# Optimization experiments

Hardware: AMD Instinct MI355X
Metric: run time of the kernel (lower is better)

## Reference

```python
import jax, jax.numpy as jnp
import numpy as np

NUM_HEADS = 4
HEAD_DIM = 32  # out_dim 128 / 4 heads


def setup_inputs() -> dict:
    key = jax.random.key(0)
    ks = jax.random.split(key, 8)
    N, E, R, D = 40000, 640000, 64, 128
    return {
        "entity_emb": jax.random.normal(ks[0], (N, D), jnp.float32),
        "relation_emb": jax.random.normal(ks[1], (R, D), jnp.float32),
        "edge_index": jax.random.randint(ks[2], (2, E), 0, N, jnp.int64),
        "edge_type": jax.random.randint(ks[3], (E,), 0, R, jnp.int64),
        "W": jax.random.normal(ks[4], (D, D), jnp.float32) / np.sqrt(D),
        "W_r": jax.random.normal(ks[5], (D, D), jnp.float32) / np.sqrt(D),
        "attn_w": jax.random.normal(ks[6], (3 * HEAD_DIM, 1), jnp.float32) / np.sqrt(3 * HEAD_DIM),
        "attn_b": jnp.zeros((1,), jnp.float32),
    }


def reference(entity_emb, relation_emb, edge_index, edge_type, W, W_r, attn_w, attn_b):
    N = entity_emb.shape[0]
    H, HD = NUM_HEADS, HEAD_DIM
    # projections (PyTorch Linear: x @ W.T)
    h = (entity_emb @ W.T).reshape(N, H, HD)
    r = relation_emb @ W_r.T
    src, dst = edge_index[0], edge_index[1]
    h_src = h[src]                                    # [E, H, HD]
    h_dst = h[dst]
    r_edge = r[edge_type].reshape(-1, H, HD)
    attn_in = jnp.concatenate([h_src, r_edge, h_dst], axis=-1)  # [E, H, 3*HD]
    scores = jax.nn.leaky_relu(attn_in @ attn_w[:, 0] + attn_b[0], negative_slope=0.2)  # [E, H]
    scores = jnp.exp(scores - jnp.max(scores))
    attn_sum = jax.ops.segment_sum(scores, dst, num_segments=N)  # [N, H]
    attn_weights = scores / (attn_sum[dst] + 1e-8)               # dropout is identity in eval
    msg = attn_weights[..., None] * h_src                        # [E, H, HD]
    out = jax.ops.segment_sum(msg, dst, num_segments=N)          # [N, H, HD]
    return out.reshape(N, H * HD)
```

## Files before the change

kernel.cpp:

```cpp
#include <hip/hip_runtime.h>
#include <math.h>

#define HEADS 4
#define DIM 128
#define CAP 128

typedef __bf16 bf16x8 __attribute__((ext_vector_type(8)));
typedef float f32x4 __attribute__((ext_vector_type(4)));

__device__ __forceinline__ unsigned short f2bf(float x) {
    unsigned u = __float_as_uint(x);
    unsigned r = (u + 0x7FFFu + ((u >> 16) & 1u)) >> 16;
    return (unsigned short)r;
}
__device__ __forceinline__ float bf2f(unsigned short v) {
    return __uint_as_float(((unsigned)v) << 16);
}

__global__ __launch_bounds__(256) void k_cvtW(const float* __restrict__ W,
                                              unsigned short* __restrict__ W16) {
    int j = blockIdx.x * 256 + threadIdx.x;
    float4 v = ((const float4*)W)[j];
    ushort4 us;
    us.x = f2bf(v.x); us.y = f2bf(v.y); us.z = f2bf(v.z); us.w = f2bf(v.w);
    ((ushort4*)W16)[j] = us;
}

__global__ __launch_bounds__(256) void k_proj(const float* __restrict__ ent,
                                              const unsigned short* __restrict__ W16,
                                              const float* __restrict__ aw,
                                              const int* __restrict__ ei,
                                              const int* __restrict__ et,
                                              unsigned short* __restrict__ h16,
                                              float4* __restrict__ s1,
                                              float4* __restrict__ s3,
                                              int* __restrict__ cnt,
                                              int* __restrict__ packed,
                                              int N, int E, int NBR) {
    int t = threadIdx.x;
    int bid = blockIdx.x;
    if (bid >= NBR) {
        int EB = gridDim.x - NBR;
        int eb = bid - NBR;
        int per = (E + EB - 1) / EB;
        int e0 = eb * per;
        int e1 = e0 + per;
        if (e1 > E) e1 = E;
        for (int e = e0 + t; e < e1; e += 256) {
            int dn = ei[E + e];
            int pos = atomicAdd(&cnt[dn], 1);
            if (pos >= CAP) pos = CAP - 1;
            packed[(size_t)dn * CAP + pos] = (ei[e] << 6) | et[e];
        }
        return;
    }
    int wv = t >> 6, lane = t & 63, ln = lane & 15, quad = lane >> 4;
    int er = bid * 64 + wv * 16 + ln;
    int erc = er < N ? er : N - 1;
    const float4* ent4 = (const float4*)ent;
    bf16x8 bfr[4];
#pragma unroll
    for (int ks = 0; ks < 4; ++ks) {
        float4 a0 = ent4[(size_t)erc * 32 + ks * 8 + quad * 2];
        float4 a1 = ent4[(size_t)erc * 32 + ks * 8 + quad * 2 + 1];
        bf16x8 f;
        f[0] = (__bf16)a0.x; f[1] = (__bf16)a0.y; f[2] = (__bf16)a0.z; f[3] = (__bf16)a0.w;
        f[4] = (__bf16)a1.x; f[5] = (__bf16)a1.y; f[6] = (__bf16)a1.z; f[7] = (__bf16)a1.w;
        bfr[ks] = f;
    }
    f32x4 acc[8];
#pragma unroll
    for (int mt = 0; mt < 8; ++mt) acc[mt] = (f32x4){0.f, 0.f, 0.f, 0.f};
#pragma unroll
    for (int ks = 0; ks < 4; ++ks) {
#pragma unroll
        for (int mt = 0; mt < 8; ++mt) {
            bf16x8 afr = *(const bf16x8*)&W16[(mt * 16 + ln) * DIM + ks * 32 + quad * 8];
            acc[mt] = __builtin_amdgcn_mfma_f32_16x16x32_bf16(afr, bfr[ks], acc[mt], 0, 0, 0);
        }
    }
    const float4* awv = (const float4*)aw;
    float s1h[4] = {0.f, 0.f, 0.f, 0.f}, s3h[4] = {0.f, 0.f, 0.f, 0.f};
#pragma unroll
    for (int mt = 0; mt < 8; ++mt) {
        int d0 = mt * 16 + quad * 4;
        if (er < N) {
            ushort4 us;
            us.x = f2bf(acc[mt][0]); us.y = f2bf(acc[mt][1]);
            us.z = f2bf(acc[mt][2]); us.w = f2bf(acc[mt][3]);
            *(ushort4*)&h16[(size_t)er * DIM + d0] = us;
        }
        int wi = (mt & 1) * 4 + quad;
        float4 w1 = awv[wi], w3 = awv[16 + wi];
        int hh = mt >> 1;
        s1h[hh] += acc[mt][0] * w1.x + acc[mt][1] * w1.y + acc[mt][2] * w1.z + acc[mt][3] * w1.w;
        s3h[hh] += acc[mt][0] * w3.x + acc[mt][1] * w3.y + acc[mt][2] * w3.z + acc[mt][3] * w3.w;
    }
#pragma unroll
    for (int hh = 0; hh < HEADS; ++hh) {
        s1h[hh] += __shfl_xor(s1h[hh], 16);
        s1h[hh] += __shfl_xor(s1h[hh], 32);
        s3h[hh] += __shfl_xor(s3h[hh], 16);
        s3h[hh] += __shfl_xor(s3h[hh], 32);
    }
    if (quad == 0 && er < N) {
        s1[er] = make_float4(s1h[0], s1h[1], s1h[2], s1h[3]);
        s3[er] = make_float4(s3h[0], s3h[1], s3h[2], s3h[3]);
    }
}

__global__ __launch_bounds__(256) void k_s2(const float* __restrict__ rel,
                                            const float* __restrict__ Wr,
                                            const float* __restrict__ aw,
                                            float* __restrict__ s2, int RH) {
    __shared__ float v[DIM * HEADS];
    int t = threadIdx.x;
    for (int i = t; i < DIM * HEADS; i += 256) {
        int k = i >> 2, hh = i & 3;
        float a = 0.f;
        for (int j = 0; j < 32; ++j) a += Wr[(hh * 32 + j) * DIM + k] * aw[32 + j];
        v[i] = a;
    }
    __syncthreads();
    int o = blockIdx.x * 4 + (t >> 6);
    if (o >= RH) return;
    int r = o >> 2, hh = o & 3;
    int l = t & 63;
    float p = rel[r * DIM + l] * v[l * 4 + hh] + rel[r * DIM + 64 + l] * v[(64 + l) * 4 + hh];
#pragma unroll
    for (int off = 32; off > 0; off >>= 1) p += __shfl_down(p, off);
    if (l == 0) s2[o] = p;
}

__global__ __launch_bounds__(64) void k_out(const int* __restrict__ packed,
                                            const int* __restrict__ cnt,
                                            const float4* __restrict__ s1,
                                            const float4* __restrict__ s2,
                                            const float4* __restrict__ s3,
                                            const float* __restrict__ ab,
                                            const unsigned short* __restrict__ h16,
                                            float* __restrict__ out, int N) {
    __shared__ int src_l[64];
    __shared__ float es_l[64 * 4];
    int n = blockIdx.x;
    int t = threadIdx.x;
    int hh = t >> 4;
    float b = ab[0];
    float4 s3n = s3[n];
    int beg = n * CAP;
    int c = cnt[n];
    if (c > CAP) c = CAP;
    float a0 = 0.f, a1 = 0.f, sum = 0.f;
    for (int base = 0; base < c; base += 64) {
        int m = c - base;
        if (m > 64) m = 64;
        __syncthreads();
        if (t < m) {
            int p = packed[beg + base + t];
            int s = p >> 6, ty = p & 63;
            float4 a = s1[s], cc = s2[ty];
            float4 sc;
            sc.x = a.x + cc.x + s3n.x + b;
            sc.y = a.y + cc.y + s3n.y + b;
            sc.z = a.z + cc.z + s3n.z + b;
            sc.w = a.w + cc.w + s3n.w + b;
            sc.x = sc.x > 0.f ? sc.x : 0.2f * sc.x;
            sc.y = sc.y > 0.f ? sc.y : 0.2f * sc.y;
            sc.z = sc.z > 0.f ? sc.z : 0.2f * sc.z;
            sc.w = sc.w > 0.f ? sc.w : 0.2f * sc.w;
            src_l[t] = s;
            es_l[t * 4 + 0] = __expf(sc.x);
            es_l[t * 4 + 1] = __expf(sc.y);
            es_l[t * 4 + 2] = __expf(sc.z);
            es_l[t * 4 + 3] = __expf(sc.w);
        }
        __syncthreads();
        int i = 0;
        for (; i + 4 <= m; i += 4) {
            int q0 = src_l[i], q1 = src_l[i + 1], q2 = src_l[i + 2], q3 = src_l[i + 3];
            float e0 = es_l[i * 4 + hh], e1 = es_l[(i + 1) * 4 + hh];
            float e2 = es_l[(i + 2) * 4 + hh], e3 = es_l[(i + 3) * 4 + hh];
            unsigned v0 = *(const unsigned*)&h16[(size_t)q0 * DIM + 2 * t];
            unsigned v1 = *(const unsigned*)&h16[(size_t)q1 * DIM + 2 * t];
            unsigned v2 = *(const unsigned*)&h16[(size_t)q2 * DIM + 2 * t];
            unsigned v3 = *(const unsigned*)&h16[(size_t)q3 * DIM + 2 * t];
            sum += (e0 + e1) + (e2 + e3);
            a0 += e0 * bf2f((unsigned short)v0);
            a1 += e0 * bf2f((unsigned short)(v0 >> 16));
            a0 += e1 * bf2f((unsigned short)v1);
            a1 += e1 * bf2f((unsigned short)(v1 >> 16));
            a0 += e2 * bf2f((unsigned short)v2);
            a1 += e2 * bf2f((unsigned short)(v2 >> 16));
            a0 += e3 * bf2f((unsigned short)v3);
            a1 += e3 * bf2f((unsigned short)(v3 >> 16));
        }
        for (; i < m; ++i) {
            int s = src_l[i];
            float e = es_l[i * 4 + hh];
            unsigned v = *(const unsigned*)&h16[(size_t)s * DIM + 2 * t];
            sum += e;
            a0 += e * bf2f((unsigned short)v);
            a1 += e * bf2f((unsigned short)(v >> 16));
        }
    }
    float inv = 1.f / (sum + 1e-8f);
    *(float2*)&out[(size_t)n * DIM + 2 * t] = make_float2(a0 * inv, a1 * inv);
}

extern "C" void kernel_launch(void* const* d_in, const int* in_sizes, int n_in,
                              void* d_out, int out_size, void* d_ws, size_t ws_size,
                              hipStream_t stream) {
    const float* ent = (const float*)d_in[0];
    const float* rel = (const float*)d_in[1];
    const int* ei = (const int*)d_in[2];
    const int* et = (const int*)d_in[3];
    const float* W = (const float*)d_in[4];
    const float* Wr = (const float*)d_in[5];
    const float* aw = (const float*)d_in[6];
    const float* ab = (const float*)d_in[7];

    int N = in_sizes[0] / DIM;
    int R = in_sizes[1] / DIM;
    int E = in_sizes[3];
    int NBR = (N + 63) / 64;
    int EB = 1875;

    char* w = (char*)d_ws;
    unsigned short* W16 = (unsigned short*)w;   w += (size_t)DIM * DIM * 2;
    unsigned short* h16 = (unsigned short*)w;   w += ((size_t)N * DIM * 2 + 15) / 16 * 16;
    float* s1 = (float*)w;     w += (size_t)N * HEADS * 4;
    float* s3 = (float*)w;     w += (size_t)N * HEADS * 4;
    float* s2 = (float*)w;     w += ((size_t)R * HEADS * 4 + 15) / 16 * 16;
    int* cnt = (int*)w;        w += (size_t)N * 4;
    int* packed = (int*)w;     w += (size_t)N * CAP * 4;

    float* out = (float*)d_out;

    (void)hipMemsetAsync(cnt, 0, (size_t)N * 4, stream);

    k_cvtW<<<16, 256, 0, stream>>>(W, W16);
    k_proj<<<NBR + EB, 256, 0, stream>>>(ent, W16, aw, ei, et, h16, (float4*)s1,
                                         (float4*)s3, cnt, packed, N, E, NBR);
    k_s2<<<(R * HEADS + 3) / 4, 256, 0, stream>>>(rel, Wr, aw, s2, R * HEADS);
    k_out<<<N, 64, 0, stream>>>(packed, cnt, (const float4*)s1, (const float4*)s2,
                                (const float4*)s3, ab, h16, out, N);
}
```

Measured before the change: 162.6 us.

## Split per-destination edge buckets into eight sub-buckets to cut atomic contention

Edge bucketing now spreads each destination's edges over 8 sub-buckets chosen by block index, each with its own counter and a capacity of 32. Each bucketing block handles a fixed 1024 edges, issuing four loads per thread before its atomics. The output kernel gathers the sub-buckets through a prefix over their counts into shared memory and does one pass with a single barrier. This aims to reduce same-address atomic contention and raise memory-level parallelism, at the cost of 8x larger counter and bucket buffers (more memset and scattered reads) and truncation if one sub-bucket receives more than 32 edges.

```diff
diff --git a/kernel.cpp b/kernel.cpp
--- a/kernel.cpp
+++ b/kernel.cpp
@@ -3,7 +3,8 @@
 
 #define HEADS 4
 #define DIM 128
-#define CAP 128
+#define NG 8
+#define CAPG 32
 
 typedef __bf16 bf16x8 __attribute__((ext_vector_type(8)));
 typedef float f32x4 __attribute__((ext_vector_type(4)));
@@ -40,18 +41,29 @@
     int t = threadIdx.x;
     int bid = blockIdx.x;
     if (bid >= NBR) {
-        int EB = gridDim.x - NBR;
+        int g = bid & (NG - 1);
         int eb = bid - NBR;
-        int per = (E + EB - 1) / EB;
-        int e0 = eb * per;
-        int e1 = e0 + per;
-        if (e1 > E) e1 = E;
-        for (int e = e0 + t; e < e1; e += 256) {
-            int dn = ei[E + e];
-            int pos = atomicAdd(&cnt[dn], 1);
-            if (pos >= CAP) pos = CAP - 1;
-            packed[(size_t)dn * CAP + pos] = (ei[e] << 6) | et[e];
+        int e0 = eb * 1024;
+        int dn[4], pk[4];
+        bool vl[4];
+#pragma unroll
+        for (int j = 0; j < 4; ++j) {
+            int e = e0 + j * 256 + t;
+            vl[j] = e < E;
+            int ec = vl[j] ? e : 0;
+            dn[j] = ei[E + ec];
+            pk[j] = (ei[ec] << 6) | et[ec];
         }
+        int pos[4];
+#pragma unroll
+        for (int j = 0; j < 4; ++j)
+            if (vl[j]) pos[j] = atomicAdd(&cnt[(size_t)g * N + dn[j]], 1);
+#pragma unroll
+        for (int j = 0; j < 4; ++j)
+            if (vl[j]) {
+                int p = pos[j] < CAPG ? pos[j] : CAPG - 1;
+                packed[((size_t)g * N + dn[j]) * CAPG + p] = pk[j];
+            }
         return;
     }
     int wv = t >> 6, lane = t & 63, ln = lane & 15, quad = lane >> 4;
@@ -140,68 +152,74 @@
                                             const float* __restrict__ ab,
                                             const unsigned short* __restrict__ h16,
                                             float* __restrict__ out, int N) {
-    __shared__ int src_l[64];
-    __shared__ float es_l[64 * 4];
+    __shared__ int src_l[NG * CAPG];
+    __shared__ float es_l[NG * CAPG * 4];
     int n = blockIdx.x;
     int t = threadIdx.x;
     int hh = t >> 4;
     float b = ab[0];
     float4 s3n = s3[n];
-    int beg = n * CAP;
-    int c = cnt[n];
-    if (c > CAP) c = CAP;
+    int cg[NG], pf[NG];
+    int tot = 0;
+#pragma unroll
+    for (int g = 0; g < NG; ++g) {
+        int c = cnt[(size_t)g * N + n];
+        if (c > CAPG) c = CAPG;
+        cg[g] = c;
+        pf[g] = tot;
+        tot += c;
+    }
+    for (int p = t; p < tot; p += 64) {
+        int g = 0;
+#pragma unroll
+        for (int gg = 1; gg < NG; ++gg)
+            if (p >= pf[gg]) g = gg;
+        int pk = packed[((size_t)g * N + n) * CAPG + (p - pf[g])];
+        int s = pk >> 6, ty = pk & 63;
+        float4 a = s1[s], cc = s2[ty];
+        float4 sc;
+        sc.x = a.x + cc.x + s3n.x + b;
+        sc.y = a.y + cc.y + s3n.y + b;
+        sc.z = a.z + cc.z + s3n.z + b;
+        sc.w = a.w + cc.w + s3n.w + b;
+        sc.x = sc.x > 0.f ? sc.x : 0.2f * sc.x;
+        sc.y = sc.y > 0.f ? sc.y : 0.2f * sc.y;
+        sc.z = sc.z > 0.f ? sc.z : 0.2f * sc.z;
+        sc.w = sc.w > 0.f ? sc.w : 0.2f * sc.w;
+        src_l[p] = s;
+        es_l[p * 4 + 0] = __expf(sc.x);
+        es_l[p * 4 + 1] = __expf(sc.y);
+        es_l[p * 4 + 2] = __expf(sc.z);
+        es_l[p * 4 + 3] = __expf(sc.w);
+    }
+    __syncthreads();
     float a0 = 0.f, a1 = 0.f, sum = 0.f;
-    for (int base = 0; base < c; base += 64) {
-        int m = c - base;
-        if (m > 64) m = 64;
-        __syncthreads();
-        if (t < m) {
-            int p = packed[beg + base + t];
-            int s = p >> 6, ty = p & 63;
-            float4 a = s1[s], cc = s2[ty];
-            float4 sc;
-            sc.x = a.x + cc.x + s3n.x + b;
-            sc.y = a.y + cc.y + s3n.y + b;
-            sc.z = a.z + cc.z + s3n.z + b;
-            sc.w = a.w + cc.w + s3n.w + b;
-            sc.x = sc.x > 0.f ? sc.x : 0.2f * sc.x;
-            sc.y = sc.y > 0.f ? sc.y : 0.2f * sc.y;
-            sc.z = sc.z > 0.f ? sc.z : 0.2f * sc.z;
-            sc.w = sc.w > 0.f ? sc.w : 0.2f * sc.w;
-            src_l[t] = s;
-            es_l[t * 4 + 0] = __expf(sc.x);
-            es_l[t * 4 + 1] = __expf(sc.y);
-            es_l[t * 4 + 2] = __expf(sc.z);
-            es_l[t * 4 + 3] = __expf(sc.w);
-        }
-        __syncthreads();
-        int i = 0;
-        for (; i + 4 <= m; i += 4) {
-            int q0 = src_l[i], q1 = src_l[i + 1], q2 = src_l[i + 2], q3 = src_l[i + 3];
-            float e0 = es_l[i * 4 + hh], e1 = es_l[(i + 1) * 4 + hh];
-            float e2 = es_l[(i + 2) * 4 + hh], e3 = es_l[(i + 3) * 4 + hh];
-            unsigned v0 = *(const unsigned*)&h16[(size_t)q0 * DIM + 2 * t];
-            unsigned v1 = *(const unsigned*)&h16[(size_t)q1 * DIM + 2 * t];
-            unsigned v2 = *(const unsigned*)&h16[(size_t)q2 * DIM + 2 * t];
-            unsigned v3 = *(const unsigned*)&h16[(size_t)q3 * DIM + 2 * t];
-            sum += (e0 + e1) + (e2 + e3);
-            a0 += e0 * bf2f((unsigned short)v0);
-            a1 += e0 * bf2f((unsigned short)(v0 >> 16));
-            a0 += e1 * bf2f((unsigned short)v1);
-            a1 += e1 * bf2f((unsigned short)(v1 >> 16));
-            a0 += e2 * bf2f((unsigned short)v2);
-            a1 += e2 * bf2f((unsigned short)(v2 >> 16));
-            a0 += e3 * bf2f((unsigned short)v3);
-            a1 += e3 * bf2f((unsigned short)(v3 >> 16));
-        }
-        for (; i < m; ++i) {
-            int s = src_l[i];
-            float e = es_l[i * 4 + hh];
-            unsigned v = *(const unsigned*)&h16[(size_t)s * DIM + 2 * t];
-            sum += e;
-            a0 += e * bf2f((unsigned short)v);
-            a1 += e * bf2f((unsigned short)(v >> 16));
-        }
+    int i = 0;
+    for (; i + 4 <= tot; i += 4) {
+        int q0 = src_l[i], q1 = src_l[i + 1], q2 = src_l[i + 2], q3 = src_l[i + 3];
+        float e0 = es_l[i * 4 + hh], e1 = es_l[(i + 1) * 4 + hh];
+        float e2 = es_l[(i + 2) * 4 + hh], e3 = es_l[(i + 3) * 4 + hh];
+        unsigned v0 = *(const unsigned*)&h16[(size_t)q0 * DIM + 2 * t];
+        unsigned v1 = *(const unsigned*)&h16[(size_t)q1 * DIM + 2 * t];
+        unsigned v2 = *(const unsigned*)&h16[(size_t)q2 * DIM + 2 * t];
+        unsigned v3 = *(const unsigned*)&h16[(size_t)q3 * DIM + 2 * t];
+        sum += (e0 + e1) + (e2 + e3);
+        a0 += e0 * bf2f((unsigned short)v0);
+        a1 += e0 * bf2f((unsigned short)(v0 >> 16));
+        a0 += e1 * bf2f((unsigned short)v1);
+        a1 += e1 * bf2f((unsigned short)(v1 >> 16));
+        a0 += e2 * bf2f((unsigned short)v2);
+        a1 += e2 * bf2f((unsigned short)(v2 >> 16));
+        a0 += e3 * bf2f((unsigned short)v3);
+        a1 += e3 * bf2f((unsigned short)(v3 >> 16));
+    }
+    for (; i < tot; ++i) {
+        int s = src_l[i];
+        float e = es_l[i * 4 + hh];
+        unsigned v = *(const unsigned*)&h16[(size_t)s * DIM + 2 * t];
+        sum += e;
+        a0 += e * bf2f((unsigned short)v);
+        a1 += e * bf2f((unsigned short)(v >> 16));
     }
     float inv = 1.f / (sum + 1e-8f);
     *(float2*)&out[(size_t)n * DIM + 2 * t] = make_float2(a0 * inv, a1 * inv);
@@ -223,7 +241,7 @@
     int R = in_sizes[1] / DIM;
     int E = in_sizes[3];
     int NBR = (N + 63) / 64;
-    int EB = 1875;
+    int EB = (E + 1023) / 1024;
 
     char* w = (char*)d_ws;
     unsigned short* W16 = (unsigned short*)w;   w += (size_t)DIM * DIM * 2;
@@ -231,12 +249,12 @@
     float* s1 = (float*)w;     w += (size_t)N * HEADS * 4;
     float* s3 = (float*)w;     w += (size_t)N * HEADS * 4;
     float* s2 = (float*)w;     w += ((size_t)R * HEADS * 4 + 15) / 16 * 16;
-    int* cnt = (int*)w;        w += (size_t)N * 4;
-    int* packed = (int*)w;     w += (size_t)N * CAP * 4;
+    int* cnt = (int*)w;        w += (size_t)NG * N * 4;
+    int* packed = (int*)w;     w += (size_t)NG * N * CAPG * 4;
 
     float* out = (float*)d_out;
 
-    (void)hipMemsetAsync(cnt, 0, (size_t)N * 4, stream);
+    (void)hipMemsetAsync(cnt, 0, (size_t)NG * N * 4, stream);
 
     k_cvtW<<<16, 256, 0, stream>>>(W, W16);
     k_proj<<<NBR + EB, 256, 0, stream>>>(ent, W16, aw, ei, et, h16, (float4*)s1,
```

Result: slower. 168.5 us (+3.6%).
